# Performance work log

Measured on AMD Instinct MI355X. Metric: run time of the kernel, lower is better.

The kernel has to match this reference:

```python
import jax, jax.numpy as jnp
import numpy as np

N_NODES = 100000
N_EDGES = 1600000
IN_FEATS = 64
HIDDEN = 64
TOPO_DIM = 16
NUM_CLASSES = 4
NUM_GRAPHS = 64


def setup_inputs() -> dict:
    key = jax.random.key(0)
    ks = jax.random.split(key, 10)
    x = jax.random.normal(ks[0], (N_NODES, IN_FEATS), dtype=jnp.float32)
    edge_index = jax.random.randint(ks[1], (2, N_EDGES), 0, N_NODES, dtype=jnp.int64)
    batch = jnp.sort(jax.random.randint(ks[2], (N_NODES,), 0, NUM_GRAPHS, dtype=jnp.int64))
    topo = jax.random.normal(ks[3], (NUM_GRAPHS, TOPO_DIM), dtype=jnp.float32)
    # GCNConv weights (glorot-ish scale) and biases
    W1 = jax.random.normal(ks[4], (IN_FEATS, HIDDEN), dtype=jnp.float32) / np.sqrt(IN_FEATS)
    b1 = jnp.zeros((HIDDEN,), dtype=jnp.float32)
    W2 = jax.random.normal(ks[5], (HIDDEN, HIDDEN), dtype=jnp.float32) / np.sqrt(HIDDEN)
    b2 = jnp.zeros((HIDDEN,), dtype=jnp.float32)
    Wlin = jax.random.normal(ks[6], (HIDDEN + TOPO_DIM, NUM_CLASSES), dtype=jnp.float32) / np.sqrt(HIDDEN + TOPO_DIM)
    blin = jnp.zeros((NUM_CLASSES,), dtype=jnp.float32)
    return {"x": x, "edge_index": edge_index, "batch": batch, "topo": topo,
            "W1": W1, "b1": b1, "W2": W2, "b2": b2, "Wlin": Wlin, "blin": blin}


def _gcn_conv(x, W, b, src, dst, deg_inv_sqrt):
    # PyG GCNConv: add self-loops, symmetric normalization D^-1/2 (A+I) D^-1/2, then linear.
    xw = x @ W                                   # [N, H]
    norm = deg_inv_sqrt[src] * deg_inv_sqrt[dst]  # [E]
    msgs = xw[src] * norm[:, None]               # gather + scale, [E, H]
    agg = jax.ops.segment_sum(msgs, dst, num_segments=x.shape[0])
    # self-loop contribution: norm_ii = deg_inv_sqrt[i]^2
    agg = agg + xw * (deg_inv_sqrt * deg_inv_sqrt)[:, None]
    return agg + b


def reference(x, edge_index, batch, topo, W1, b1, W2, b2, Wlin, blin):
    src, dst = edge_index[0], edge_index[1]
    n = x.shape[0]
    # degree including self-loop
    deg = jax.ops.segment_sum(jnp.ones_like(dst, dtype=x.dtype), dst, num_segments=n) + 1.0
    deg_inv_sqrt = jax.lax.rsqrt(deg)
    h = jax.nn.relu(_gcn_conv(x, W1, b1, src, dst, deg_inv_sqrt))
    # F.dropout(p=0.5, training=False) -> identity at inference
    h = jax.nn.relu(_gcn_conv(h, W2, b2, src, dst, deg_inv_sqrt))
    # global mean pool over graphs
    sums = jax.ops.segment_sum(h, batch, num_segments=NUM_GRAPHS)
    counts = jax.ops.segment_sum(jnp.ones((n,), dtype=h.dtype), batch, num_segments=NUM_GRAPHS)
    g = sums / jnp.maximum(counts, 1.0)[:, None]  # [G, H]
    gtopo = jnp.concatenate([g, topo], axis=1)    # [G, H + topo_dim]
    return gtopo @ Wlin + blin
```

## Files before the change

### kernel.cpp

```cpp
#include <hip/hip_runtime.h>
#include <hip/hip_bf16.h>

#define NGRAPH  64
#define TOPO_D  16
#define NBLK    512
#define MAXB    512
#define GROWS   8
#define PCH     16

typedef float v2f __attribute__((ext_vector_type(2)));

static __device__ __forceinline__ unsigned short f2bf(float f) {
    unsigned u = __float_as_uint(f);
    unsigned r = (u + 0x7FFFu + ((u >> 16) & 1u)) >> 16;
    return (unsigned short)r;
}
static __device__ __forceinline__ float bf_lo(unsigned u) { return __uint_as_float(u << 16); }
static __device__ __forceinline__ float bf_hi(unsigned u) { return __uint_as_float(u & 0xFFFF0000u); }

static __device__ __forceinline__ void gemm_rows_bf(
        const float* __restrict__ X, const float* Wreg,
        unsigned short* __restrict__ Abf, int row0, int N, int lane) {
    #pragma unroll
    for (int j = 0; j < GROWS; ++j) {
        int row = row0 + j;
        if (row >= N) return;
        const float* xr = X + (size_t)row * 64;
        float acc = 0.0f;
        #pragma unroll
        for (int k = 0; k < 64; ++k) acc = fmaf(xr[k], Wreg[k], acc);
        Abf[(size_t)row * 64 + lane] = f2bf(acc);
    }
}

static __device__ __forceinline__ void gemm_rows_fp8(
        const float* __restrict__ X, const float* Wreg,
        unsigned* __restrict__ A8, const float* __restrict__ dis,
        int row0, int N, int lane) {
    #pragma unroll
    for (int j = 0; j < GROWS; ++j) {
        int row = row0 + j;
        if (row >= N) return;
        const float* xr = X + (size_t)row * 64;
        float acc = 0.0f;
        #pragma unroll
        for (int k = 0; k < 64; ++k) acc = fmaf(xr[k], Wreg[k], acc);
        acc *= dis[row];
        float nb1 = __shfl_xor(acc, 1, 64);
        float lo = (lane & 1) ? nb1 : acc;
        float hi = (lane & 1) ? acc : nb1;
        int pk = __builtin_amdgcn_cvt_pk_fp8_f32(lo, hi, 0, false);
        int pk2 = __shfl_xor(pk, 2, 64);
        unsigned dw = (lane & 2) ? (((unsigned)pk2 & 0xFFFFu) | ((unsigned)pk << 16))
                                 : (((unsigned)pk & 0xFFFFu) | ((unsigned)pk2 << 16));
        if ((lane & 3) == 0) A8[(size_t)row * 16 + (lane >> 2)] = dw;
    }
}

__global__ __launch_bounds__(256) void hybrid_gemm_hist_kernel(
        const float* __restrict__ X, const float* __restrict__ W,
        unsigned short* __restrict__ Abf,
        const int* __restrict__ dst, int* __restrict__ bhist,
        int N, int E, int Gg, int nb2, int CE) {
    __shared__ int hist[MAXB];
    int t = threadIdx.x;
    if ((int)blockIdx.x < Gg) {
        int lane = t & 63;
        float Wreg[64];
        #pragma unroll
        for (int k = 0; k < 64; ++k) Wreg[k] = W[k * 64 + lane];
        int wave = __builtin_amdgcn_readfirstlane(blockIdx.x * 4 + (t >> 6));
        gemm_rows_bf(X, Wreg, Abf, wave * GROWS, N, lane);
    } else {
        int blk = blockIdx.x - Gg;
        for (int i = t; i < nb2; i += 256) hist[i] = 0;
        __syncthreads();
        int e0 = blk * CE, e1 = min(e0 + CE, E);
        for (int e = e0 + t; e < e1; e += 256) atomicAdd(&hist[dst[e] >> 8], 1);
        __syncthreads();
        for (int i = t; i < nb2; i += 256) bhist[blk * nb2 + i] = hist[i];
    }
}

__global__ __launch_bounds__(256) void scan_cols_kernel(
        int* __restrict__ bhist, int* __restrict__ ctot, int nb2) {
    __shared__ int sd[256];
    int c = blockIdx.x;
    int t = threadIdx.x;
    int v0 = bhist[t * nb2 + c];
    int v1 = bhist[(t + 256) * nb2 + c];
    int tsum = v0 + v1;
    sd[t] = tsum; __syncthreads();
    for (int off = 1; off < 256; off <<= 1) {
        int u = (t >= off) ? sd[t - off] : 0;
        __syncthreads();
        sd[t] += u;
        __syncthreads();
    }
    int excl = sd[t] - tsum;
    bhist[t * nb2 + c] = excl;
    bhist[(t + 256) * nb2 + c] = excl + v0;
    if (t == 255) ctot[c] = sd[255];
}

__global__ void scan_gstart_kernel(const int* __restrict__ ctot, int* __restrict__ cbase,
                                   const int* __restrict__ batch, int* __restrict__ gstart,
                                   int nb2, int N) {
    if (blockIdx.x == 0) {
        int lane = threadIdx.x;
        if (lane >= 64) return;
        int base = lane * 8;
        int vals[8];
        int s = 0;
        #pragma unroll
        for (int k = 0; k < 8; ++k) {
            int i = base + k;
            int v = (i < nb2) ? ctot[i] : 0;
            vals[k] = s; s += v;
        }
        int inc = s;
        for (int off = 1; off < 64; off <<= 1) {
            int u = __shfl_up(inc, off, 64);
            if (lane >= off) inc += u;
        }
        int lexcl = inc - s;
        #pragma unroll
        for (int k = 0; k < 8; ++k) {
            int i = base + k;
            if (i <= nb2) cbase[i] = lexcl + vals[k];
        }
    } else {
        int g = threadIdx.x;
        if (g > NGRAPH) return;
        int lo = 0, hi = N;
        while (lo < hi) {
            int mid = (lo + hi) >> 1;
            if (batch[mid] < g) lo = mid + 1; else hi = mid;
        }
        gstart[g] = lo;
    }
}

__global__ __launch_bounds__(256) void scatter_sorted_kernel(
        const int* __restrict__ src, const int* __restrict__ dst,
        const int* __restrict__ bhist, const int* __restrict__ cbase,
        unsigned* __restrict__ ebuf, int E, int nb2, int CE) {
    __shared__ int cur[MAXB];
    int blk = blockIdx.x, t = threadIdx.x;
    for (int i = t; i < nb2; i += 256) cur[i] = bhist[blk * nb2 + i] + cbase[i];
    __syncthreads();
    int e0 = blk * CE, e1 = min(e0 + CE, E);
    for (int e = e0 + t; e < e1; e += 256) {
        int d = dst[e];
        int pos = atomicAdd(&cur[d >> 8], 1);
        ebuf[pos] = ((unsigned)src[e] << 8) | (unsigned)(d & 255);
    }
}

__global__ __launch_bounds__(256) void build_csr_kernel(
        const unsigned* __restrict__ ebuf, const int* __restrict__ cbase,
        int* __restrict__ col, int* __restrict__ rowptr,
        int* __restrict__ degi, float* __restrict__ dis,
        const unsigned* __restrict__ Abf32, unsigned* __restrict__ A8, int N) {
    __shared__ int cnt[256];
    __shared__ int loff[256];
    __shared__ float disS[256];
    int b = blockIdx.x, t = threadIdx.x;
    int e0 = cbase[b], e1 = cbase[b + 1];
    cnt[t] = 0; __syncthreads();
    for (int i = e0 + t; i < e1; i += 256) atomicAdd(&cnt[ebuf[i] & 255u], 1);
    __syncthreads();
    int v = cnt[t];
    loff[t] = v; __syncthreads();
    for (int off = 1; off < 256; off <<= 1) {
        int u = (t >= off) ? loff[t - off] : 0;
        __syncthreads();
        loff[t] += u;
        __syncthreads();
    }
    int excl = loff[t] - v;
    int node = b * 256 + t;
    float ds = rsqrtf((float)v + 1.0f);
    disS[t] = ds;
    if (node < N) {
        degi[node]   = v;
        dis[node]    = ds;
        rowptr[node] = e0 + excl;
    }
    __syncthreads();
    cnt[t] = excl;
    __syncthreads();
    for (int i = e0 + t; i < e1; i += 256) {
        unsigned p = ebuf[i];
        int pos = atomicAdd(&cnt[p & 255u], 1);
        col[e0 + pos] = (int)(p >> 8);
    }
    int base8 = b * 256 * 16;
    for (int i = t; i < 256 * 16; i += 256) {
        int r = i >> 4;
        int dwo = i & 15;
        int nd = b * 256 + r;
        if (nd < N) {
            float d2 = disS[r];
            unsigned u0 = Abf32[(size_t)nd * 32 + dwo * 2];
            unsigned u1 = Abf32[(size_t)nd * 32 + dwo * 2 + 1];
            int dw = __builtin_amdgcn_cvt_pk_fp8_f32(bf_lo(u0) * d2, bf_hi(u0) * d2, 0, false);
            dw = __builtin_amdgcn_cvt_pk_fp8_f32(bf_lo(u1) * d2, bf_hi(u1) * d2, dw, true);
            A8[base8 + i] = (unsigned)dw;
        }
    }
}

__global__ __launch_bounds__(256) void pull_csr_kernel(
        const unsigned* __restrict__ A8, float* __restrict__ B,
        const int* __restrict__ rowptr, const int* __restrict__ degi,
        const float* __restrict__ dis, const float* __restrict__ bias,
        const int* __restrict__ col, int N) {
    int wave = (blockIdx.x * blockDim.x + threadIdx.x) >> 6;
    int lane = threadIdx.x & 63;
    int i = lane >> 3;
    int f8 = lane & 7;
    int node = wave * 8 + i;
    bool valid = node < N;
    if (!valid) node = N - 1;
    int deg = degi[node];
    int beg = rowptr[node];
    const char* Abase = (const char*)A8 + f8 * 8;
    uint2 an = *(const uint2*)(Abase + ((size_t)node << 6));
    v2f a0 = __builtin_amdgcn_cvt_pk_f32_fp8(an.x, false);
    v2f a1 = __builtin_amdgcn_cvt_pk_f32_fp8(an.x, true);
    v2f a2 = __builtin_amdgcn_cvt_pk_f32_fp8(an.y, false);
    v2f a3 = __builtin_amdgcn_cvt_pk_f32_fp8(an.y, true);
    float acc[8] = {a0.x, a0.y, a1.x, a1.y, a2.x, a2.y, a3.x, a3.y};
    int j = 0;
    for (; j + 4 <= deg; j += 4) {
        int s0 = col[beg + j]     << 6;
        int s1 = col[beg + j + 1] << 6;
        int s2 = col[beg + j + 2] << 6;
        int s3 = col[beg + j + 3] << 6;
        uint2 v0 = *(const uint2*)(Abase + s0);
        uint2 v1 = *(const uint2*)(Abase + s1);
        uint2 v2 = *(const uint2*)(Abase + s2);
        uint2 v3 = *(const uint2*)(Abase + s3);
        v2f f0, f1, f2, f3;
        f0 = __builtin_amdgcn_cvt_pk_f32_fp8(v0.x, false); acc[0] += f0.x; acc[1] += f0.y;
        f1 = __builtin_amdgcn_cvt_pk_f32_fp8(v0.x, true);  acc[2] += f1.x; acc[3] += f1.y;
        f2 = __builtin_amdgcn_cvt_pk_f32_fp8(v0.y, false); acc[4] += f2.x; acc[5] += f2.y;
        f3 = __builtin_amdgcn_cvt_pk_f32_fp8(v0.y, true);  acc[6] += f3.x; acc[7] += f3.y;
        f0 = __builtin_amdgcn_cvt_pk_f32_fp8(v1.x, false); acc[0] += f0.x; acc[1] += f0.y;
        f1 = __builtin_amdgcn_cvt_pk_f32_fp8(v1.x, true);  acc[2] += f1.x; acc[3] += f1.y;
        f2 = __builtin_amdgcn_cvt_pk_f32_fp8(v1.y, false); acc[4] += f2.x; acc[5] += f2.y;
        f3 = __builtin_amdgcn_cvt_pk_f32_fp8(v1.y, true);  acc[6] += f3.x; acc[7] += f3.y;
        f0 = __builtin_amdgcn_cvt_pk_f32_fp8(v2.x, false); acc[0] += f0.x; acc[1] += f0.y;
        f1 = __builtin_amdgcn_cvt_pk_f32_fp8(v2.x, true);  acc[2] += f1.x; acc[3] += f1.y;
        f2 = __builtin_amdgcn_cvt_pk_f32_fp8(v2.y, false); acc[4] += f2.x; acc[5] += f2.y;
        f3 = __builtin_amdgcn_cvt_pk_f32_fp8(v2.y, true);  acc[6] += f3.x; acc[7] += f3.y;
        f0 = __builtin_amdgcn_cvt_pk_f32_fp8(v3.x, false); acc[0] += f0.x; acc[1] += f0.y;
        f1 = __builtin_amdgcn_cvt_pk_f32_fp8(v3.x, true);  acc[2] += f1.x; acc[3] += f1.y;
        f2 = __builtin_amdgcn_cvt_pk_f32_fp8(v3.y, false); acc[4] += f2.x; acc[5] += f2.y;
        f3 = __builtin_amdgcn_cvt_pk_f32_fp8(v3.y, true);  acc[6] += f3.x; acc[7] += f3.y;
    }
    for (; j < deg; ++j) {
        int s = col[beg + j] << 6;
        uint2 v = *(const uint2*)(Abase + s);
        v2f f0 = __builtin_amdgcn_cvt_pk_f32_fp8(v.x, false);
        v2f f1 = __builtin_amdgcn_cvt_pk_f32_fp8(v.x, true);
        v2f f2 = __builtin_amdgcn_cvt_pk_f32_fp8(v.y, false);
        v2f f3 = __builtin_amdgcn_cvt_pk_f32_fp8(v.y, true);
        acc[0] += f0.x; acc[1] += f0.y; acc[2] += f1.x; acc[3] += f1.y;
        acc[4] += f2.x; acc[5] += f2.y; acc[6] += f3.x; acc[7] += f3.y;
    }
    float d = dis[node];
    float4 b0 = ((const float4*)bias)[f8 * 2];
    float4 b1 = ((const float4*)bias)[f8 * 2 + 1];
    float4 r0, r1;
    r0.x = fmaxf(d * acc[0] + b0.x, 0.f);
    r0.y = fmaxf(d * acc[1] + b0.y, 0.f);
    r0.z = fmaxf(d * acc[2] + b0.z, 0.f);
    r0.w = fmaxf(d * acc[3] + b0.w, 0.f);
    r1.x = fmaxf(d * acc[4] + b1.x, 0.f);
    r1.y = fmaxf(d * acc[5] + b1.y, 0.f);
    r1.z = fmaxf(d * acc[6] + b1.z, 0.f);
    r1.w = fmaxf(d * acc[7] + b1.w, 0.f);
    if (valid) {
        *(float4*)(B + (size_t)node * 64 + f8 * 8)     = r0;
        *(float4*)(B + (size_t)node * 64 + f8 * 8 + 4) = r1;
    }
}

__global__ __launch_bounds__(256) void gemm_scale_kernel(
        const float* __restrict__ X, const float* __restrict__ W,
        const float* __restrict__ dis, unsigned* __restrict__ A8, int N) {
    int lane = threadIdx.x & 63;
    float Wreg[64];
    #pragma unroll
    for (int k = 0; k < 64; ++k) Wreg[k] = W[k * 64 + lane];
    int wave = __builtin_amdgcn_readfirstlane(blockIdx.x * 4 + (threadIdx.x >> 6));
    gemm_rows_fp8(X, Wreg, A8, dis, wave * GROWS, N, lane);
}

__global__ __launch_bounds__(256) void pool2_kernel(
        const float* __restrict__ H, const int* __restrict__ gstart,
        float* __restrict__ gsum) {
    __shared__ float red[4][64];
    int b = blockIdx.x;
    int g = b >> 4;
    int c = b & 15;
    int s = gstart[g], e = gstart[g + 1];
    int len = e - s;
    int chunk = (len + PCH - 1) / PCH;
    int lo = s + c * chunk;
    int hi = min(lo + chunk, e);
    int w = threadIdx.x >> 6;
    int lane = threadIdx.x & 63;
    float acc0 = 0.f, acc1 = 0.f;
    int n = lo + w;
    for (; n + 4 < hi; n += 8) {
        acc0 += H[(size_t)n * 64 + lane];
        acc1 += H[(size_t)(n + 4) * 64 + lane];
    }
    if (n < hi) acc0 += H[(size_t)n * 64 + lane];
    red[w][lane] = acc0 + acc1;
    __syncthreads();
    if (threadIdx.x < 64) {
        float v = red[0][threadIdx.x] + red[1][threadIdx.x]
                + red[2][threadIdx.x] + red[3][threadIdx.x];
        unsafeAtomicAdd(&gsum[g * 64 + threadIdx.x], v);
    }
}

__global__ __launch_bounds__(256) void head_kernel(
        const float* __restrict__ gsum, const int* __restrict__ gstart,
        const float* __restrict__ topo, const float* __restrict__ Wlin,
        const float* __restrict__ blin, float* __restrict__ out) {
    int t = threadIdx.x;
    int g = t >> 2;
    int c = t & 3;
    float cntf = (float)(gstart[g + 1] - gstart[g]);
    float inv = 1.0f / fmaxf(cntf, 1.0f);
    float v = blin[c];
    #pragma unroll
    for (int f = 0; f < 64; ++f) v += gsum[g * 64 + f] * inv * Wlin[f * 4 + c];
    #pragma unroll
    for (int t2 = 0; t2 < TOPO_D; ++t2) v += topo[g * TOPO_D + t2] * Wlin[(64 + t2) * 4 + c];
    out[g * 4 + c] = v;
}

extern "C" void kernel_launch(void* const* d_in, const int* in_sizes, int n_in,
                              void* d_out, int out_size, void* d_ws, size_t ws_size,
                              hipStream_t stream) {
    const float* x     = (const float*)d_in[0];
    const int*   ei    = (const int*)d_in[1];
    const int*   batch = (const int*)d_in[2];
    const float* topo  = (const float*)d_in[3];
    const float* W1    = (const float*)d_in[4];
    const float* b1    = (const float*)d_in[5];
    const float* W2    = (const float*)d_in[6];
    const float* b2    = (const float*)d_in[7];
    const float* Wlin  = (const float*)d_in[8];
    const float* blin  = (const float*)d_in[9];
    float* out = (float*)d_out;

    const int N = in_sizes[0] / 64;
    const int E = in_sizes[1] / 2;
    const int* src = ei;
    const int* dst = ei + E;
    const int nb2 = (N + 255) / 256;
    const int CE  = (E + NBLK - 1) / NBLK;

    char* ws = (char*)d_ws;
    size_t off = 0;
    unsigned short* Abf = (unsigned short*)(ws + off); off += (size_t)N * 64 * 2;
    unsigned* A8     = (unsigned*)(ws + off); off += (size_t)N * 64;
    float*    B      = (float*)   (ws + off); off += (size_t)N * 64 * 4;
    int*      col    = (int*)     (ws + off); off += (size_t)E * 4;
    unsigned* ebuf   = (unsigned*)(ws + off); off += (size_t)E * 4;
    int*      bhist  = (int*)     (ws + off); off += (size_t)NBLK * nb2 * 4;
    int*      ctot   = (int*)     (ws + off); off += (size_t)(nb2 + 8) * 4;
    int*      cbase  = (int*)     (ws + off); off += (size_t)(nb2 + 8) * 4;
    int*      rowptr = (int*)     (ws + off); off += (size_t)(N + 1) * 4;
    int*      degi   = (int*)     (ws + off); off += (size_t)N * 4;
    float*    dis    = (float*)   (ws + off); off += (size_t)N * 4;
    int*      gstart = (int*)     (ws + off); off += (size_t)(NGRAPH + 8) * 4;
    float*    gsum   = (float*)   (ws + off); off += (size_t)NGRAPH * 64 * 4;

    hipMemsetAsync(gsum, 0, (size_t)NGRAPH * 64 * 4, stream);

    const int nWaves = (N + GROWS - 1) / GROWS;
    const int Gg = (nWaves + 3) / 4;
    hybrid_gemm_hist_kernel<<<Gg + NBLK, 256, 0, stream>>>(x, W1, Abf, dst, bhist, N, E, Gg, nb2, CE);
    scan_cols_kernel<<<nb2, 256, 0, stream>>>(bhist, ctot, nb2);
    scan_gstart_kernel<<<2, 256, 0, stream>>>(ctot, cbase, batch, gstart, nb2, N);
    scatter_sorted_kernel<<<NBLK, 256, 0, stream>>>(src, dst, bhist, cbase, ebuf, E, nb2, CE);
    build_csr_kernel<<<nb2, 256, 0, stream>>>(ebuf, cbase, col, rowptr, degi, dis,
                                              (const unsigned*)Abf, A8, N);

    int pullBlocks = ((N + 7) / 8 + 3) / 4;
    pull_csr_kernel<<<pullBlocks, 256, 0, stream>>>(A8, B, rowptr, degi, dis, b1, col, N);

    gemm_scale_kernel<<<Gg, 256, 0, stream>>>(B, W2, dis, A8, N);
    pull_csr_kernel<<<pullBlocks, 256, 0, stream>>>(A8, B, rowptr, degi, dis, b2, col, N);

    pool2_kernel<<<NGRAPH * PCH, 256, 0, stream>>>(B, gstart, gsum);
    head_kernel<<<1, 256, 0, stream>>>(gsum, gstart, topo, Wlin, blin, out);
}
```

Baseline: 250.2 us.

## Fuse second GCN aggregation with global mean pooling via shared-memory atomics

```diff
diff --git a/kernel.cpp b/kernel.cpp
--- a/kernel.cpp
+++ b/kernel.cpp
@@ -6,7 +6,7 @@
 #define NBLK    512
 #define MAXB    512
 #define GROWS   8
-#define PCH     16
+#define GSPAN   8
 
 typedef float v2f __attribute__((ext_vector_type(2)));
 
@@ -211,27 +211,17 @@
     }
 }
 
-__global__ __launch_bounds__(256) void pull_csr_kernel(
-        const unsigned* __restrict__ A8, float* __restrict__ B,
-        const int* __restrict__ rowptr, const int* __restrict__ degi,
-        const float* __restrict__ dis, const float* __restrict__ bias,
-        const int* __restrict__ col, int N) {
-    int wave = (blockIdx.x * blockDim.x + threadIdx.x) >> 6;
-    int lane = threadIdx.x & 63;
-    int i = lane >> 3;
-    int f8 = lane & 7;
-    int node = wave * 8 + i;
-    bool valid = node < N;
-    if (!valid) node = N - 1;
-    int deg = degi[node];
-    int beg = rowptr[node];
+static __device__ __forceinline__ void gather_node(
+        const unsigned* __restrict__ A8, const int* __restrict__ col,
+        int beg, int deg, int node, int f8, float acc[8]) {
     const char* Abase = (const char*)A8 + f8 * 8;
     uint2 an = *(const uint2*)(Abase + ((size_t)node << 6));
     v2f a0 = __builtin_amdgcn_cvt_pk_f32_fp8(an.x, false);
     v2f a1 = __builtin_amdgcn_cvt_pk_f32_fp8(an.x, true);
     v2f a2 = __builtin_amdgcn_cvt_pk_f32_fp8(an.y, false);
     v2f a3 = __builtin_amdgcn_cvt_pk_f32_fp8(an.y, true);
-    float acc[8] = {a0.x, a0.y, a1.x, a1.y, a2.x, a2.y, a3.x, a3.y};
+    acc[0] = a0.x; acc[1] = a0.y; acc[2] = a1.x; acc[3] = a1.y;
+    acc[4] = a2.x; acc[5] = a2.y; acc[6] = a3.x; acc[7] = a3.y;
     int j = 0;
     for (; j + 4 <= deg; j += 4) {
         int s0 = col[beg + j]     << 6;
@@ -270,6 +260,24 @@
         acc[0] += f0.x; acc[1] += f0.y; acc[2] += f1.x; acc[3] += f1.y;
         acc[4] += f2.x; acc[5] += f2.y; acc[6] += f3.x; acc[7] += f3.y;
     }
+}
+
+__global__ __launch_bounds__(256) void pull_csr_kernel(
+        const unsigned* __restrict__ A8, float* __restrict__ B,
+        const int* __restrict__ rowptr, const int* __restrict__ degi,
+        const float* __restrict__ dis, const float* __restrict__ bias,
+        const int* __restrict__ col, int N) {
+    int wave = (blockIdx.x * blockDim.x + threadIdx.x) >> 6;
+    int lane = threadIdx.x & 63;
+    int i = lane >> 3;
+    int f8 = lane & 7;
+    int node = wave * 8 + i;
+    bool valid = node < N;
+    if (!valid) node = N - 1;
+    int deg = degi[node];
+    int beg = rowptr[node];
+    float acc[8];
+    gather_node(A8, col, beg, deg, node, f8, acc);
     float d = dis[node];
     float4 b0 = ((const float4*)bias)[f8 * 2];
     float4 b1 = ((const float4*)bias)[f8 * 2 + 1];
@@ -288,6 +296,63 @@
     }
 }
 
+__global__ __launch_bounds__(256) void pull_pool_kernel(
+        const unsigned* __restrict__ A8,
+        const int* __restrict__ rowptr, const int* __restrict__ degi,
+        const float* __restrict__ dis, const float* __restrict__ bias,
+        const int* __restrict__ col, const int* __restrict__ batch,
+        float* __restrict__ gsum, int N) {
+    __shared__ float gacc[GSPAN * 64];
+    int t = threadIdx.x;
+    for (int k = t; k < GSPAN * 64; k += 256) gacc[k] = 0.f;
+    int n0 = blockIdx.x * 32;
+    int g0 = batch[min(n0, N - 1)];
+    int span = batch[min(n0 + 31, N - 1)] - g0;
+    __syncthreads();
+    int wave = (blockIdx.x * blockDim.x + threadIdx.x) >> 6;
+    int lane = t & 63;
+    int i = lane >> 3;
+    int f8 = lane & 7;
+    int node = wave * 8 + i;
+    bool valid = node < N;
+    if (!valid) node = N - 1;
+    int deg = degi[node];
+    int beg = rowptr[node];
+    float acc[8];
+    gather_node(A8, col, beg, deg, node, f8, acc);
+    float d = dis[node];
+    float4 b0 = ((const float4*)bias)[f8 * 2];
+    float4 b1 = ((const float4*)bias)[f8 * 2 + 1];
+    float r[8];
+    r[0] = fmaxf(d * acc[0] + b0.x, 0.f);
+    r[1] = fmaxf(d * acc[1] + b0.y, 0.f);
+    r[2] = fmaxf(d * acc[2] + b0.z, 0.f);
+    r[3] = fmaxf(d * acc[3] + b0.w, 0.f);
+    r[4] = fmaxf(d * acc[4] + b1.x, 0.f);
+    r[5] = fmaxf(d * acc[5] + b1.y, 0.f);
+    r[6] = fmaxf(d * acc[6] + b1.z, 0.f);
+    r[7] = fmaxf(d * acc[7] + b1.w, 0.f);
+    if (valid) {
+        int g = batch[node];
+        if (span < GSPAN) {
+            int base = (g - g0) * 64 + f8 * 8;
+            #pragma unroll
+            for (int c = 0; c < 8; ++c) atomicAdd(&gacc[base + c], r[c]);
+        } else {
+            #pragma unroll
+            for (int c = 0; c < 8; ++c) unsafeAtomicAdd(&gsum[g * 64 + f8 * 8 + c], r[c]);
+        }
+    }
+    __syncthreads();
+    if (span < GSPAN) {
+        int lim = (span + 1) * 64;
+        for (int k = t; k < lim; k += 256) {
+            float v = gacc[k];
+            if (v != 0.f) unsafeAtomicAdd(&gsum[g0 * 64 + k], v);
+        }
+    }
+}
+
 __global__ __launch_bounds__(256) void gemm_scale_kernel(
         const float* __restrict__ X, const float* __restrict__ W,
         const float* __restrict__ dis, unsigned* __restrict__ A8, int N) {
@@ -297,36 +362,6 @@
     for (int k = 0; k < 64; ++k) Wreg[k] = W[k * 64 + lane];
     int wave = __builtin_amdgcn_readfirstlane(blockIdx.x * 4 + (threadIdx.x >> 6));
     gemm_rows_fp8(X, Wreg, A8, dis, wave * GROWS, N, lane);
-}
-
-__global__ __launch_bounds__(256) void pool2_kernel(
-        const float* __restrict__ H, const int* __restrict__ gstart,
-        float* __restrict__ gsum) {
-    __shared__ float red[4][64];
-    int b = blockIdx.x;
-    int g = b >> 4;
-    int c = b & 15;
-    int s = gstart[g], e = gstart[g + 1];
-    int len = e - s;
-    int chunk = (len + PCH - 1) / PCH;
-    int lo = s + c * chunk;
-    int hi = min(lo + chunk, e);
-    int w = threadIdx.x >> 6;
-    int lane = threadIdx.x & 63;
-    float acc0 = 0.f, acc1 = 0.f;
-    int n = lo + w;
-    for (; n + 4 < hi; n += 8) {
-        acc0 += H[(size_t)n * 64 + lane];
-        acc1 += H[(size_t)(n + 4) * 64 + lane];
-    }
-    if (n < hi) acc0 += H[(size_t)n * 64 + lane];
-    red[w][lane] = acc0 + acc1;
-    __syncthreads();
-    if (threadIdx.x < 64) {
-        float v = red[0][threadIdx.x] + red[1][threadIdx.x]
-                + red[2][threadIdx.x] + red[3][threadIdx.x];
-        unsafeAtomicAdd(&gsum[g * 64 + threadIdx.x], v);
-    }
 }
 
 __global__ __launch_bounds__(256) void head_kernel(
@@ -399,8 +434,8 @@
     pull_csr_kernel<<<pullBlocks, 256, 0, stream>>>(A8, B, rowptr, degi, dis, b1, col, N);
 
     gemm_scale_kernel<<<Gg, 256, 0, stream>>>(B, W2, dis, A8, N);
-    pull_csr_kernel<<<pullBlocks, 256, 0, stream>>>(A8, B, rowptr, degi, dis, b2, col, N);
-
-    pool2_kernel<<<NGRAPH * PCH, 256, 0, stream>>>(B, gstart, gsum);
+    pull_pool_kernel<<<pullBlocks, 256, 0, stream>>>(A8, rowptr, degi, dis, b2, col,
+                                                     batch, gsum, N);
+
     head_kernel<<<1, 256, 0, stream>>>(gsum, gstart, topo, Wlin, blin, out);
 }
```

Result: slower. 267.3 us (+6.9%).
